# Performance work log

Measured on AMD Instinct MI355X. Metric: run time of the kernel, lower is better.

The kernel has to match this reference:

```python
import jax, jax.numpy as jnp
import numpy as np

EPS = 1e-3  # BatchNorm eps from module

def _bn(x, g, b, m, v):
    # torch BatchNorm1d (eval): (x - mean) / sqrt(var + eps) * weight + bias
    return (x - m) * (g / jnp.sqrt(v + EPS)) + b

def setup_inputs() -> dict:
    key = jax.random.key(0)
    ks = jax.random.split(key, 16)
    N, Cin, Cout, S = 1_000_000, 16, 64, 20_000
    inputs = jax.random.normal(ks[0], (N, Cin), dtype=jnp.float32)
    unq_inv = jax.random.randint(ks[1], (N,), 0, S, dtype=jnp.int32)

    def bn_params(k, c):
        k1, k2, k3, k4 = jax.random.split(k, 4)
        return (1.0 + 0.01 * jax.random.normal(k1, (c,), jnp.float32),
                0.01 * jax.random.normal(k2, (c,), jnp.float32),
                0.01 * jax.random.normal(k3, (c,), jnp.float32),
                jax.random.uniform(k4, (c,), jnp.float32, 0.5, 1.5))

    W1 = 0.1 * jax.random.normal(ks[2], (Cin, Cout), jnp.float32)
    g1, b1, m1, v1 = bn_params(ks[3], Cout)
    W2a = 0.1 * jax.random.normal(ks[4], (Cin, 2 * Cout), jnp.float32)
    g2a, b2a, m2a, v2a = bn_params(ks[5], 2 * Cout)
    W2b = 0.1 * jax.random.normal(ks[6], (2 * Cout, Cout), jnp.float32)
    g2b, b2b, m2b, v2b = bn_params(ks[7], Cout)

    return dict(inputs=inputs, unq_inv=unq_inv, num_segments=S,
                W1=W1, g1=g1, b1=b1, m1=m1, v1=v1,
                W2a=W2a, g2a=g2a, b2a=b2a, m2a=m2a, v2a=v2a,
                W2b=W2b, g2b=b2b * 0 + g2b, b2b=b2b, m2b=m2b, v2b=v2b)

def reference(inputs, unq_inv, num_segments,
              W1, g1, b1, m1, v1,
              W2a, g2a, b2a, m2a, v2a,
              W2b, g2b, b2b, m2b, v2b):
    # branch 1: Linear -> BN -> ReLU
    x = jax.nn.relu(_bn(inputs @ W1, g1, b1, m1, v1))            # [N, C]
    # branch 2: Linear -> BN -> ReLU -> Linear -> BN -> ReLU
    h = jax.nn.relu(_bn(inputs @ W2a, g2a, b2a, m2a, v2a))       # [N, 2C]
    x2 = jax.nn.relu(_bn(h @ W2b, g2b, b2b, m2b, v2b))           # [N, C]

    # segment reductions over group ids
    x_max = jax.ops.segment_max(x, unq_inv, num_segments=num_segments)  # [S, C]
    x_max = jnp.maximum(x_max, 0.0)  # empty segments -> 0 (x >= 0 post-ReLU)
    group_sum = jax.ops.segment_sum(x, unq_inv, num_segments=num_segments)  # [S, C]
    max_pool = jnp.max(x2, axis=0)                                # [C], global pool
    max_pool = jnp.broadcast_to(max_pool[None, :], x_max.shape)   # [S, C]

    feat = jnp.concatenate((group_sum, x_max, max_pool), axis=1)  # [S, 3C]
    # channel shuffle with groups=3
    S_, C3 = feat.shape
    feat = feat.reshape(S_, 3, C3 // 3).transpose(0, 2, 1).reshape(S_, C3)
    return feat
```

## Files before the change

kernel.cpp:

```cpp
#include <hip/hip_runtime.h>

#define EPS 1e-3f

#define OFF_T2B    7168
#define OFF_MPP    7232
#define OFF_CNT    11328
#define OFF_OFFS   31344
#define OFF_CUR    51360
#define OFF_INPS   71424

typedef short short8 __attribute__((ext_vector_type(8)));
typedef float f32x4 __attribute__((ext_vector_type(4)));

union U4 { unsigned u[4]; short8 s8; };

__device__ inline unsigned short f2bf(float f) {
    unsigned u = __float_as_uint(f);
    return (unsigned short)((u + 0x7FFFu + ((u >> 16) & 1u)) >> 16);
}

__global__ __launch_bounds__(256) void setup_k(
    const float* __restrict__ W1,
    const float* __restrict__ g1, const float* __restrict__ b1,
    const float* __restrict__ m1, const float* __restrict__ v1,
    const float* __restrict__ W2a,
    const float* __restrict__ g2a, const float* __restrict__ b2a,
    const float* __restrict__ m2a, const float* __restrict__ v2a,
    const float* __restrict__ W2b,
    const float* __restrict__ g2b, const float* __restrict__ b2b,
    const float* __restrict__ m2b, const float* __restrict__ v2b,
    unsigned short* __restrict__ wsu, float* __restrict__ wsf)
{
    const int t = threadIdx.x;
    for (int i = t; i < 64 * 32; i += 256) {
        int ch = i >> 5, k = i & 31;
        float s = g1[ch] * rsqrtf(v1[ch] + EPS);
        float val = (k < 16) ? W1[k * 64 + ch] * s
                  : (k == 16 ? b1[ch] - m1[ch] * s : 0.f);
        wsu[i] = f2bf(val);
    }
    for (int i = t; i < 128 * 32; i += 256) {
        int ch = i >> 5, k = i & 31;
        float s = g2a[ch] * rsqrtf(v2a[ch] + EPS);
        float val = (k < 16) ? W2a[k * 128 + ch] * s
                  : (k == 16 ? b2a[ch] - m2a[ch] * s : 0.f);
        wsu[2048 + i] = f2bf(val);
    }
    for (int i = t; i < 64 * 128; i += 256) {
        int ch = i >> 7, k = i & 127;
        float s = g2b[ch] * rsqrtf(v2b[ch] + EPS);
        wsu[2048 + 4096 + i] = f2bf(W2b[k * 64 + ch] * s);
    }
    if (t < 64) {
        float s = g2b[t] * rsqrtf(v2b[t] + EPS);
        wsf[OFF_T2B + t] = b2b[t] - m2b[t] * s;
    }
}

__global__ __launch_bounds__(256) void hist_k(
    const int* __restrict__ unq, int* __restrict__ cnt, int N)
{
    const int i = blockIdx.x * 256 + threadIdx.x;
    if (i < N) atomicAdd(&cnt[unq[i]], 1);
}

__global__ __launch_bounds__(1024) void scan_k(
    const int* __restrict__ cnt, int* __restrict__ offs,
    int* __restrict__ cur, int S)
{
    __shared__ int tot[1024];
    const int t = threadIdx.x;
    const int E = (S + 1023) >> 10;
    const int i0 = t * E;
    int run = 0;
    for (int j = 0; j < E; ++j) {
        const int i = i0 + j;
        run += (i < S) ? cnt[i] : 0;
    }
    tot[t] = run;
    __syncthreads();
    for (int d = 1; d < 1024; d <<= 1) {
        int x = (t >= d) ? tot[t - d] : 0;
        __syncthreads();
        tot[t] += x;
        __syncthreads();
    }
    int base = (t == 0) ? 0 : tot[t - 1];
    for (int j = 0; j < E; ++j) {
        const int i = i0 + j;
        if (i < S) {
            offs[i] = base;
            cur[i]  = base;
            base += cnt[i];
        }
    }
    if (t == 1023) offs[S] = tot[1023];
}

__global__ __launch_bounds__(512, 2) void scatbr2_k(
    const float* __restrict__ inputs,
    const int*   __restrict__ unq,
    int*         __restrict__ cur,
    uint4*       __restrict__ inpS,
    const uint4* __restrict__ wsw,
    const float* __restrict__ wsf,
    float* __restrict__ mpp,
    int N)
{
    __shared__ __align__(16) char w2as[8192];
    __shared__ __align__(16) char w2bs[16384];
    __shared__ float t2bs[64];
    __shared__ float mpb[64];
    __shared__ __align__(16) char scrs[8][4096];

    const int tid = threadIdx.x;
    {
        int u = tid;
        *reinterpret_cast<uint4*>(&w2as[(u * 16) ^ (((u >> 2) & 7) << 4)]) = wsw[256 + u];
        for (int v = tid; v < 1024; v += 512)
            *reinterpret_cast<uint4*>(&w2bs[(v * 16) ^ (((v >> 4) & 7) << 4)]) = wsw[768 + v];
        if (tid < 64) { t2bs[tid] = wsf[OFF_T2B + tid]; mpb[tid] = 0.f; }
    }
    __syncthreads();

    const int wv   = tid >> 6;
    const int lane = tid & 63;
    const int c = lane & 15;
    const int g = lane >> 4;
    const unsigned swz = (unsigned)(lane & 7) << 4;
    char* scr = scrs[wv];

    const long wave_pt0 = (long)blockIdx.x * 512 + wv * 64;
    const long i  = wave_pt0 + lane;
    const bool lane_ok = (i < N);
    const long idx = lane_ok ? i : (long)(N - 1);
    const long nrem_w = (long)N - wave_pt0;

    unsigned pk[8];
    {
        const float4* p = reinterpret_cast<const float4*>(inputs + idx * 16);
        float4 a0 = p[0], a1 = p[1], a2 = p[2], a3 = p[3];
        asm("v_cvt_pk_bf16_f32 %0, %1, %2" : "=v"(pk[0]) : "v"(a0.x), "v"(a0.y));
        asm("v_cvt_pk_bf16_f32 %0, %1, %2" : "=v"(pk[1]) : "v"(a0.z), "v"(a0.w));
        asm("v_cvt_pk_bf16_f32 %0, %1, %2" : "=v"(pk[2]) : "v"(a1.x), "v"(a1.y));
        asm("v_cvt_pk_bf16_f32 %0, %1, %2" : "=v"(pk[3]) : "v"(a1.z), "v"(a1.w));
        asm("v_cvt_pk_bf16_f32 %0, %1, %2" : "=v"(pk[4]) : "v"(a2.x), "v"(a2.y));
        asm("v_cvt_pk_bf16_f32 %0, %1, %2" : "=v"(pk[5]) : "v"(a2.z), "v"(a2.w));
        asm("v_cvt_pk_bf16_f32 %0, %1, %2" : "=v"(pk[6]) : "v"(a3.x), "v"(a3.y));
        asm("v_cvt_pk_bf16_f32 %0, %1, %2" : "=v"(pk[7]) : "v"(a3.z), "v"(a3.w));
        if (!lane_ok) {
            #pragma unroll
            for (int j = 0; j < 8; ++j) pk[j] = 0u;
        }
    }
    if (lane_ok) {
        const int seg = unq[idx];
        const int pos = atomicAdd(&cur[seg], 1);
        inpS[(size_t)pos * 2]     = make_uint4(pk[0], pk[1], pk[2], pk[3]);
        inpS[(size_t)pos * 2 + 1] = make_uint4(pk[4], pk[5], pk[6], pk[7]);
    }

    f32x4 t2br[4];
    #pragma unroll
    for (int mt = 0; mt < 4; ++mt)
        t2br[mt] = *reinterpret_cast<const f32x4*>(&t2bs[mt * 16 + g * 4]);

    const f32x4 zero4 = {0.f, 0.f, 0.f, 0.f};
    float mp[16];
    #pragma unroll
    for (int j = 0; j < 16; ++j) mp[j] = 0.f;

    for (int ti = 0; ti < 4; ++ti) {
        if ((long)ti * 16 >= nrem_w) break;
        const bool act = (long)(ti * 16 + c) < nrem_w;

        U4 bf;
        {
            const int src = ti * 16 + c;
            unsigned s0 = (unsigned)__shfl((int)pk[0], src, 64);
            unsigned s1 = (unsigned)__shfl((int)pk[1], src, 64);
            unsigned s2 = (unsigned)__shfl((int)pk[2], src, 64);
            unsigned s3 = (unsigned)__shfl((int)pk[3], src, 64);
            unsigned s4 = (unsigned)__shfl((int)pk[4], src, 64);
            unsigned s5 = (unsigned)__shfl((int)pk[5], src, 64);
            unsigned s6 = (unsigned)__shfl((int)pk[6], src, 64);
            unsigned s7 = (unsigned)__shfl((int)pk[7], src, 64);
            bool ghi = (lane & 16) != 0;
            bf.u[0] = ghi ? s4 : s0;
            bf.u[1] = ghi ? s5 : s1;
            bf.u[2] = ghi ? s6 : s2;
            bf.u[3] = ghi ? s7 : s3;
            if (lane >= 32) {
                bf.u[0] = (lane < 48 && act) ? 0x00003F80u : 0u;
                bf.u[1] = 0u; bf.u[2] = 0u; bf.u[3] = 0u;
            }
        }

        #pragma unroll
        for (int mt = 0; mt < 8; ++mt) {
            short8 a = *reinterpret_cast<const short8*>(
                &w2as[(unsigned)((mt * 16 + c) * 64 + g * 16) ^ swz]);
            f32x4 hT = __builtin_amdgcn_mfma_f32_16x16x32_bf16(a, bf.s8, zero4, 0, 0, 0);
            float h0 = fmaxf(hT[0], 0.f), h1 = fmaxf(hT[1], 0.f);
            float h2 = fmaxf(hT[2], 0.f), h3 = fmaxf(hT[3], 0.f);
            unsigned lo, hi;
            asm("v_cvt_pk_bf16_f32 %0, %1, %2" : "=v"(lo) : "v"(h0), "v"(h1));
            asm("v_cvt_pk_bf16_f32 %0, %1, %2" : "=v"(hi) : "v"(h2), "v"(h3));
            *reinterpret_cast<uint2*>(
                &scr[(unsigned)(c * 256 + mt * 32 + g * 8) ^ swz]) = make_uint2(lo, hi);
        }
        __builtin_amdgcn_wave_barrier();
        asm volatile("s_waitcnt lgkmcnt(0)" ::: "memory");
        __builtin_amdgcn_sched_barrier(0);

        f32x4 y2t[4];
        #pragma unroll
        for (int mt = 0; mt < 4; ++mt) y2t[mt] = zero4;
        #pragma unroll
        for (int ks = 0; ks < 4; ++ks) {
            short8 hb = *reinterpret_cast<const short8*>(
                &scr[(unsigned)(c * 256 + ks * 64 + g * 16) ^ swz]);
            #pragma unroll
            for (int mt = 0; mt < 4; ++mt) {
                short8 a = *reinterpret_cast<const short8*>(
                    &w2bs[(unsigned)((mt * 16 + c) * 256 + ks * 64 + g * 16) ^ swz]);
                y2t[mt] = __builtin_amdgcn_mfma_f32_16x16x32_bf16(a, hb, y2t[mt], 0, 0, 0);
            }
        }
        #pragma unroll
        for (int mt = 0; mt < 4; ++mt) {
            #pragma unroll
            for (int r = 0; r < 4; ++r) {
                float v = fmaxf(y2t[mt][r] + t2br[mt][r], 0.f);
                if (act) mp[mt * 4 + r] = fmaxf(mp[mt * 4 + r], v);
            }
        }
        __builtin_amdgcn_wave_barrier();
        asm volatile("s_waitcnt lgkmcnt(0)" ::: "memory");
        __builtin_amdgcn_sched_barrier(0);
    }

    #pragma unroll
    for (int j = 0; j < 16; ++j) {
        float x = mp[j];
        x = fmaxf(x, __shfl_xor(x, 1, 64));
        x = fmaxf(x, __shfl_xor(x, 2, 64));
        x = fmaxf(x, __shfl_xor(x, 4, 64));
        x = fmaxf(x, __shfl_xor(x, 8, 64));
        mp[j] = x;
    }
    if (c == 0) {
        #pragma unroll
        for (int mt = 0; mt < 4; ++mt)
            #pragma unroll
            for (int r = 0; r < 4; ++r)
                atomicMax(reinterpret_cast<int*>(&mpb[mt * 16 + g * 4 + r]),
                          __float_as_int(mp[mt * 4 + r]));
    }
    __syncthreads();
    if (tid < 64)
        atomicMax(reinterpret_cast<int*>(mpp + (blockIdx.x & 63) * 64 + tid),
                  __float_as_int(mpb[tid]));
}

__global__ __launch_bounds__(512) void seg1_k(
    const uint4* __restrict__ inpS,
    const int*   __restrict__ offs,
    const uint4* __restrict__ wsw,
    const float* __restrict__ mpp,
    float* __restrict__ out,
    int S, int Npt)
{
    __shared__ __align__(16) char w1s[4096];
    __shared__ float mps[64];
    __shared__ float scr3[8][192];

    const int tid = threadIdx.x;
    if (tid < 256) {
        int u = tid;
        *reinterpret_cast<uint4*>(&w1s[(u * 16) ^ (((u >> 2) & 7) << 4)]) = wsw[u];
    }
    if (tid < 64) {
        float m = 0.f;
        #pragma unroll
        for (int s = 0; s < 64; ++s)
            m = fmaxf(m, mpp[s * 64 + tid]);
        mps[tid] = m;
    }
    __syncthreads();

    const int wv   = tid >> 6;
    const int lane = tid & 63;
    const int seg  = blockIdx.x * 8 + wv;
    if (seg >= S) return;

    const int c = lane & 15;
    const int g = lane >> 4;
    const unsigned swz = (unsigned)(lane & 7) << 4;

    const int start = offs[seg];
    const int end   = offs[seg + 1];

    const f32x4 zero4 = {0.f, 0.f, 0.f, 0.f};
    f32x4 as[4], am[4];
    #pragma unroll
    for (int mt = 0; mt < 4; ++mt) { as[mt] = zero4; am[mt] = zero4; }

    for (int base = start; base < end; base += 64) {
        const int nrem = end - base;
        #pragma unroll
        for (int ti = 0; ti < 4; ++ti) {
            if (ti * 16 >= nrem) break;
            const bool act = (ti * 16 + c) < nrem;
            int row = base + ti * 16 + c;
            row = min(row, Npt - 1);

            U4 bf;
            {
                uint4 q = inpS[(size_t)row * 2 + (g & 1)];
                const bool data = (g < 2) && act;
                bf.u[0] = data ? q.x : ((g == 2 && act) ? 0x00003F80u : 0u);
                bf.u[1] = data ? q.y : 0u;
                bf.u[2] = data ? q.z : 0u;
                bf.u[3] = data ? q.w : 0u;
            }
            #pragma unroll
            for (int mt = 0; mt < 4; ++mt) {
                short8 a = *reinterpret_cast<const short8*>(
                    &w1s[(unsigned)((mt * 16 + c) * 64 + g * 16) ^ swz]);
                f32x4 y1t = __builtin_amdgcn_mfma_f32_16x16x32_bf16(a, bf.s8, zero4, 0, 0, 0);
                #pragma unroll
                for (int r = 0; r < 4; ++r) {
                    float v = fmaxf(y1t[r], 0.f);
                    as[mt][r] += v;
                    am[mt][r]  = fmaxf(am[mt][r], v);
                }
            }
        }
    }

    #pragma unroll
    for (int mt = 0; mt < 4; ++mt) {
        #pragma unroll
        for (int r = 0; r < 4; ++r) {
            float xs = as[mt][r], xm = am[mt][r];
            xs += __shfl_xor(xs, 1, 64);  xm = fmaxf(xm, __shfl_xor(xm, 1, 64));
            xs += __shfl_xor(xs, 2, 64);  xm = fmaxf(xm, __shfl_xor(xm, 2, 64));
            xs += __shfl_xor(xs, 4, 64);  xm = fmaxf(xm, __shfl_xor(xm, 4, 64));
            xs += __shfl_xor(xs, 8, 64);  xm = fmaxf(xm, __shfl_xor(xm, 8, 64));
            as[mt][r] = xs; am[mt][r] = xm;
        }
    }

    float* sr = scr3[wv];
    if (c == 0) {
        #pragma unroll
        for (int mt = 0; mt < 4; ++mt)
            #pragma unroll
            for (int r = 0; r < 4; ++r) {
                const int ch = mt * 16 + g * 4 + r;
                sr[ch * 3 + 0] = as[mt][r];
                sr[ch * 3 + 1] = am[mt][r];
            }
    }
    sr[lane * 3 + 2] = mps[lane];
    __builtin_amdgcn_wave_barrier();
    asm volatile("s_waitcnt lgkmcnt(0)" ::: "memory");
    __builtin_amdgcn_sched_barrier(0);

    float* o = out + (size_t)seg * 192;
    #pragma unroll
    for (int p = 0; p < 3; ++p)
        o[p * 64 + lane] = sr[p * 64 + lane];
}

extern "C" void kernel_launch(void* const* d_in, const int* in_sizes, int n_in,
                              void* d_out, int out_size, void* d_ws, size_t ws_size,
                              hipStream_t stream)
{
    const float* inputs = (const float*)d_in[0];
    const int*   unq    = (const int*)d_in[1];
    const float* W1  = (const float*)d_in[3];
    const float* g1  = (const float*)d_in[4];
    const float* b1  = (const float*)d_in[5];
    const float* m1  = (const float*)d_in[6];
    const float* v1  = (const float*)d_in[7];
    const float* W2a = (const float*)d_in[8];
    const float* g2a = (const float*)d_in[9];
    const float* b2a = (const float*)d_in[10];
    const float* m2a = (const float*)d_in[11];
    const float* v2a = (const float*)d_in[12];
    const float* W2b = (const float*)d_in[13];
    const float* g2b = (const float*)d_in[14];
    const float* b2b = (const float*)d_in[15];
    const float* m2b = (const float*)d_in[16];
    const float* v2b = (const float*)d_in[17];

    float* wsf = (float*)d_ws;
    float* out = (float*)d_out;
    const int N = in_sizes[0] / 16;
    const int S = out_size / 192;

    float* mpp  = wsf + OFF_MPP;
    int*   cnt  = (int*)(wsf + OFF_CNT);
    int*   offs = (int*)(wsf + OFF_OFFS);
    int*   cur  = (int*)(wsf + OFF_CUR);
    uint4* inpS = (uint4*)(wsf + OFF_INPS);

    hipMemsetAsync(mpp, 0, (size_t)(OFF_CNT + 20016 - OFF_MPP) * sizeof(float), stream);

    setup_k<<<1, 256, 0, stream>>>(W1, g1, b1, m1, v1,
                                   W2a, g2a, b2a, m2a, v2a,
                                   W2b, g2b, b2b, m2b, v2b,
                                   (unsigned short*)d_ws, wsf);

    hist_k<<<(N + 255) / 256, 256, 0, stream>>>(unq, cnt, N);
    scan_k<<<1, 1024, 0, stream>>>(cnt, offs, cur, S);

    scatbr2_k<<<(N + 511) / 512, 512, 0, stream>>>(inputs, unq, cur, inpS,
                                                   (const uint4*)d_ws, wsf, mpp, N);

    seg1_k<<<(S + 7) / 8, 512, 0, stream>>>(inpS, offs, (const uint4*)d_ws,
                                            mpp, out, S, N);
}
```

Baseline: 218.0 us.

## Merge setup and histogram kernels; load inputs per MFMA tile instead of shuffles

Folds the one-block weight setup kernel into the histogram kernel, using block 0 for setup, which removes one launch and lets setup overlap with the histogram. In the scatter/branch-2 kernel, each lane now loads its bf16 input fragment directly per 16-row tile instead of loading a full row and broadcasting it with eight shuffles. The scatter atomic is done by one lane group and its position is broadcast by shuffle. Explicit wave barriers and lgkmcnt waits around the scratch LDS exchange are removed, and the tile loop is unrolled. Removing those waits risks LDS read-after-write ordering relying on compiler-inserted waits, and the inputs are now loaded in smaller scattered chunks.

```diff
diff --git a/kernel.cpp b/kernel.cpp
--- a/kernel.cpp
+++ b/kernel.cpp
@@ -19,7 +19,7 @@
     return (unsigned short)((u + 0x7FFFu + ((u >> 16) & 1u)) >> 16);
 }
 
-__global__ __launch_bounds__(256) void setup_k(
+__global__ __launch_bounds__(256) void init_k(
     const float* __restrict__ W1,
     const float* __restrict__ g1, const float* __restrict__ b1,
     const float* __restrict__ m1, const float* __restrict__ v1,
@@ -29,39 +29,38 @@
     const float* __restrict__ W2b,
     const float* __restrict__ g2b, const float* __restrict__ b2b,
     const float* __restrict__ m2b, const float* __restrict__ v2b,
-    unsigned short* __restrict__ wsu, float* __restrict__ wsf)
+    unsigned short* __restrict__ wsu, float* __restrict__ wsf,
+    const int* __restrict__ unq, int* __restrict__ cnt, int N)
 {
     const int t = threadIdx.x;
-    for (int i = t; i < 64 * 32; i += 256) {
-        int ch = i >> 5, k = i & 31;
-        float s = g1[ch] * rsqrtf(v1[ch] + EPS);
-        float val = (k < 16) ? W1[k * 64 + ch] * s
-                  : (k == 16 ? b1[ch] - m1[ch] * s : 0.f);
-        wsu[i] = f2bf(val);
-    }
-    for (int i = t; i < 128 * 32; i += 256) {
-        int ch = i >> 5, k = i & 31;
-        float s = g2a[ch] * rsqrtf(v2a[ch] + EPS);
-        float val = (k < 16) ? W2a[k * 128 + ch] * s
-                  : (k == 16 ? b2a[ch] - m2a[ch] * s : 0.f);
-        wsu[2048 + i] = f2bf(val);
-    }
-    for (int i = t; i < 64 * 128; i += 256) {
-        int ch = i >> 7, k = i & 127;
-        float s = g2b[ch] * rsqrtf(v2b[ch] + EPS);
-        wsu[2048 + 4096 + i] = f2bf(W2b[k * 64 + ch] * s);
-    }
-    if (t < 64) {
-        float s = g2b[t] * rsqrtf(v2b[t] + EPS);
-        wsf[OFF_T2B + t] = b2b[t] - m2b[t] * s;
-    }
-}
-
-__global__ __launch_bounds__(256) void hist_k(
-    const int* __restrict__ unq, int* __restrict__ cnt, int N)
-{
-    const int i = blockIdx.x * 256 + threadIdx.x;
-    if (i < N) atomicAdd(&cnt[unq[i]], 1);
+    if (blockIdx.x == 0) {
+        for (int i = t; i < 64 * 32; i += 256) {
+            int ch = i >> 5, k = i & 31;
+            float s = g1[ch] * rsqrtf(v1[ch] + EPS);
+            float val = (k < 16) ? W1[k * 64 + ch] * s
+                      : (k == 16 ? b1[ch] - m1[ch] * s : 0.f);
+            wsu[i] = f2bf(val);
+        }
+        for (int i = t; i < 128 * 32; i += 256) {
+            int ch = i >> 5, k = i & 31;
+            float s = g2a[ch] * rsqrtf(v2a[ch] + EPS);
+            float val = (k < 16) ? W2a[k * 128 + ch] * s
+                      : (k == 16 ? b2a[ch] - m2a[ch] * s : 0.f);
+            wsu[2048 + i] = f2bf(val);
+        }
+        for (int i = t; i < 64 * 128; i += 256) {
+            int ch = i >> 7, k = i & 127;
+            float s = g2b[ch] * rsqrtf(v2b[ch] + EPS);
+            wsu[2048 + 4096 + i] = f2bf(W2b[k * 64 + ch] * s);
+        }
+        if (t < 64) {
+            float s = g2b[t] * rsqrtf(v2b[t] + EPS);
+            wsf[OFF_T2B + t] = b2b[t] - m2b[t] * s;
+        }
+    } else {
+        const int i = (blockIdx.x - 1) * 256 + t;
+        if (i < N) atomicAdd(&cnt[unq[i]], 1);
+    }
 }
 
 __global__ __launch_bounds__(1024) void scan_k(
@@ -130,35 +129,8 @@
     const unsigned swz = (unsigned)(lane & 7) << 4;
     char* scr = scrs[wv];
 
-    const long wave_pt0 = (long)blockIdx.x * 512 + wv * 64;
-    const long i  = wave_pt0 + lane;
-    const bool lane_ok = (i < N);
-    const long idx = lane_ok ? i : (long)(N - 1);
+    const long wave_pt0 = (long)blockIdx.x * 512 + (long)wv * 64;
     const long nrem_w = (long)N - wave_pt0;
-
-    unsigned pk[8];
-    {
-        const float4* p = reinterpret_cast<const float4*>(inputs + idx * 16);
-        float4 a0 = p[0], a1 = p[1], a2 = p[2], a3 = p[3];
-        asm("v_cvt_pk_bf16_f32 %0, %1, %2" : "=v"(pk[0]) : "v"(a0.x), "v"(a0.y));
-        asm("v_cvt_pk_bf16_f32 %0, %1, %2" : "=v"(pk[1]) : "v"(a0.z), "v"(a0.w));
-        asm("v_cvt_pk_bf16_f32 %0, %1, %2" : "=v"(pk[2]) : "v"(a1.x), "v"(a1.y));
-        asm("v_cvt_pk_bf16_f32 %0, %1, %2" : "=v"(pk[3]) : "v"(a1.z), "v"(a1.w));
-        asm("v_cvt_pk_bf16_f32 %0, %1, %2" : "=v"(pk[4]) : "v"(a2.x), "v"(a2.y));
-        asm("v_cvt_pk_bf16_f32 %0, %1, %2" : "=v"(pk[5]) : "v"(a2.z), "v"(a2.w));
-        asm("v_cvt_pk_bf16_f32 %0, %1, %2" : "=v"(pk[6]) : "v"(a3.x), "v"(a3.y));
-        asm("v_cvt_pk_bf16_f32 %0, %1, %2" : "=v"(pk[7]) : "v"(a3.z), "v"(a3.w));
-        if (!lane_ok) {
-            #pragma unroll
-            for (int j = 0; j < 8; ++j) pk[j] = 0u;
-        }
-    }
-    if (lane_ok) {
-        const int seg = unq[idx];
-        const int pos = atomicAdd(&cur[seg], 1);
-        inpS[(size_t)pos * 2]     = make_uint4(pk[0], pk[1], pk[2], pk[3]);
-        inpS[(size_t)pos * 2 + 1] = make_uint4(pk[4], pk[5], pk[6], pk[7]);
-    }
 
     f32x4 t2br[4];
     #pragma unroll
@@ -170,31 +142,32 @@
     #pragma unroll
     for (int j = 0; j < 16; ++j) mp[j] = 0.f;
 
+    #pragma unroll
     for (int ti = 0; ti < 4; ++ti) {
         if ((long)ti * 16 >= nrem_w) break;
         const bool act = (long)(ti * 16 + c) < nrem_w;
+        const long pt  = wave_pt0 + ti * 16 + c;
 
         U4 bf;
-        {
-            const int src = ti * 16 + c;
-            unsigned s0 = (unsigned)__shfl((int)pk[0], src, 64);
-            unsigned s1 = (unsigned)__shfl((int)pk[1], src, 64);
-            unsigned s2 = (unsigned)__shfl((int)pk[2], src, 64);
-            unsigned s3 = (unsigned)__shfl((int)pk[3], src, 64);
-            unsigned s4 = (unsigned)__shfl((int)pk[4], src, 64);
-            unsigned s5 = (unsigned)__shfl((int)pk[5], src, 64);
-            unsigned s6 = (unsigned)__shfl((int)pk[6], src, 64);
-            unsigned s7 = (unsigned)__shfl((int)pk[7], src, 64);
-            bool ghi = (lane & 16) != 0;
-            bf.u[0] = ghi ? s4 : s0;
-            bf.u[1] = ghi ? s5 : s1;
-            bf.u[2] = ghi ? s6 : s2;
-            bf.u[3] = ghi ? s7 : s3;
-            if (lane >= 32) {
-                bf.u[0] = (lane < 48 && act) ? 0x00003F80u : 0u;
-                bf.u[1] = 0u; bf.u[2] = 0u; bf.u[3] = 0u;
-            }
-        }
+        if (g < 2) {
+            const long row = act ? pt : (long)(N - 1);
+            const float4* p = reinterpret_cast<const float4*>(inputs + row * 16 + g * 8);
+            float4 f0 = p[0], f1 = p[1];
+            asm("v_cvt_pk_bf16_f32 %0, %1, %2" : "=v"(bf.u[0]) : "v"(f0.x), "v"(f0.y));
+            asm("v_cvt_pk_bf16_f32 %0, %1, %2" : "=v"(bf.u[1]) : "v"(f0.z), "v"(f0.w));
+            asm("v_cvt_pk_bf16_f32 %0, %1, %2" : "=v"(bf.u[2]) : "v"(f1.x), "v"(f1.y));
+            asm("v_cvt_pk_bf16_f32 %0, %1, %2" : "=v"(bf.u[3]) : "v"(f1.z), "v"(f1.w));
+            if (!act) { bf.u[0] = 0u; bf.u[1] = 0u; bf.u[2] = 0u; bf.u[3] = 0u; }
+        } else {
+            bf.u[0] = (g == 2 && act) ? 0x00003F80u : 0u;
+            bf.u[1] = 0u; bf.u[2] = 0u; bf.u[3] = 0u;
+        }
+
+        int pos = 0;
+        if (g == 0 && act) pos = atomicAdd(&cur[unq[pt]], 1);
+        pos = __shfl(pos, c, 64);
+        if (g < 2 && act)
+            inpS[(size_t)pos * 2 + g] = make_uint4(bf.u[0], bf.u[1], bf.u[2], bf.u[3]);
 
         #pragma unroll
         for (int mt = 0; mt < 8; ++mt) {
@@ -209,9 +182,6 @@
             *reinterpret_cast<uint2*>(
                 &scr[(unsigned)(c * 256 + mt * 32 + g * 8) ^ swz]) = make_uint2(lo, hi);
         }
-        __builtin_amdgcn_wave_barrier();
-        asm volatile("s_waitcnt lgkmcnt(0)" ::: "memory");
-        __builtin_amdgcn_sched_barrier(0);
 
         f32x4 y2t[4];
         #pragma unroll
@@ -235,9 +205,6 @@
                 if (act) mp[mt * 4 + r] = fmaxf(mp[mt * 4 + r], v);
             }
         }
-        __builtin_amdgcn_wave_barrier();
-        asm volatile("s_waitcnt lgkmcnt(0)" ::: "memory");
-        __builtin_amdgcn_sched_barrier(0);
     }
 
     #pragma unroll
@@ -312,17 +279,18 @@
         for (int ti = 0; ti < 4; ++ti) {
             if (ti * 16 >= nrem) break;
             const bool act = (ti * 16 + c) < nrem;
-            int row = base + ti * 16 + c;
-            row = min(row, Npt - 1);
 
             U4 bf;
-            {
-                uint4 q = inpS[(size_t)row * 2 + (g & 1)];
-                const bool data = (g < 2) && act;
-                bf.u[0] = data ? q.x : ((g == 2 && act) ? 0x00003F80u : 0u);
-                bf.u[1] = data ? q.y : 0u;
-                bf.u[2] = data ? q.z : 0u;
-                bf.u[3] = data ? q.w : 0u;
+            if (g < 2) {
+                int row = min(base + ti * 16 + c, Npt - 1);
+                uint4 q = inpS[(size_t)row * 2 + g];
+                bf.u[0] = act ? q.x : 0u;
+                bf.u[1] = act ? q.y : 0u;
+                bf.u[2] = act ? q.z : 0u;
+                bf.u[3] = act ? q.w : 0u;
+            } else {
+                bf.u[0] = (g == 2 && act) ? 0x00003F80u : 0u;
+                bf.u[1] = 0u; bf.u[2] = 0u; bf.u[3] = 0u;
             }
             #pragma unroll
             for (int mt = 0; mt < 4; ++mt) {
@@ -409,12 +377,10 @@
 
     hipMemsetAsync(mpp, 0, (size_t)(OFF_CNT + 20016 - OFF_MPP) * sizeof(float), stream);
 
-    setup_k<<<1, 256, 0, stream>>>(W1, g1, b1, m1, v1,
-                                   W2a, g2a, b2a, m2a, v2a,
-                                   W2b, g2b, b2b, m2b, v2b,
-                                   (unsigned short*)d_ws, wsf);
-
-    hist_k<<<(N + 255) / 256, 256, 0, stream>>>(unq, cnt, N);
+    init_k<<<1 + (N + 255) / 256, 256, 0, stream>>>(
+        W1, g1, b1, m1, v1, W2a, g2a, b2a, m2a, v2a, W2b, g2b, b2b, m2b, v2b,
+        (unsigned short*)d_ws, wsf, unq, cnt, N);
+
     scan_k<<<1, 1024, 0, stream>>>(cnt, offs, cur, S);
 
     scatbr2_k<<<(N + 511) / 512, 512, 0, stream>>>(inputs, unq, cur, inpS,
```

New measurement: 205.7 us. -5.6%, faster.
